# Kernel tuning notes

Hardware: AMD Instinct MI355X
Metric: run time of the kernel (lower is better)

The kernel has to match this reference:

```python
import jax, jax.numpy as jnp
import numpy as np

N = 50000
IN_C, HID_C, OUT_C = 128, 64, 32
E = 800000
NEG_SLOPE = 0.2


def setup_inputs() -> dict:
    key = jax.random.key(0)
    ks = jax.random.split(key, 8)
    x = jax.random.normal(ks[0], (N, IN_C), dtype=jnp.float32)
    edge_index = jax.random.randint(ks[1], (2, E), 0, N, dtype=jnp.int64)
    # GATConv params (heads=1): lin weight, att_src/att_dst vectors, bias
    sc = 1.0 / np.sqrt(IN_C)
    W = jax.random.uniform(ks[2], (IN_C, HID_C), jnp.float32, -sc, sc)
    att_src = jax.random.normal(ks[3], (HID_C,), jnp.float32) * (1.0 / np.sqrt(HID_C))
    att_dst = jax.random.normal(ks[4], (HID_C,), jnp.float32) * (1.0 / np.sqrt(HID_C))
    bias_conv = jnp.zeros((HID_C,), jnp.float32)
    sl = 1.0 / np.sqrt(HID_C)
    W_lin = jax.random.uniform(ks[5], (HID_C, OUT_C), jnp.float32, -sl, sl)
    b_lin = jax.random.uniform(ks[6], (OUT_C,), jnp.float32, -sl, sl)
    return {"x": x, "edge_index": edge_index, "W": W, "att_src": att_src,
            "att_dst": att_dst, "bias_conv": bias_conv, "W_lin": W_lin, "b_lin": b_lin}


def reference(x, edge_index, W, att_src, att_dst, bias_conv, W_lin, b_lin):
    n = x.shape[0]
    h = x @ W  # [N, HID]
    # add self-loops (PyG GATConv default add_self_loops=True)
    loop = jnp.arange(n, dtype=edge_index.dtype)
    src = jnp.concatenate([edge_index[0], loop])  # [E+N]
    dst = jnp.concatenate([edge_index[1], loop])
    a_src = h @ att_src  # [N]
    a_dst = h @ att_dst
    e = jax.nn.leaky_relu(a_src[src] + a_dst[dst], NEG_SLOPE)  # [E+N]
    # segment softmax over incoming edges per destination node
    m = jax.ops.segment_max(e, dst, num_segments=n)
    e = jnp.exp(e - m[dst])
    denom = jax.ops.segment_sum(e, dst, num_segments=n)
    alpha = e / (denom[dst] + 1e-16)
    msg = alpha[:, None] * h[src]  # [E+N, HID]
    out = jax.ops.segment_sum(msg, dst, num_segments=n) + bias_conv
    out = jax.nn.relu(out)
    return out @ W_lin + b_lin
```

## Files before the change

kernel.cpp:

```cpp
#include <hip/hip_runtime.h>
#include <hip/hip_bf16.h>

#define IN_C  128
#define HID_C 64
#define OUT_C 32
#define NEG_SLOPE 0.2f
#define EPB1    2048
#define BUCKETW 32
#define RCAP    768
#define SUPW    1024
#define RCAP1   18432
#define CSTRIDE 16
#define XS_LD   136

typedef short bf16x8 __attribute__((ext_vector_type(8)));
typedef float f32x4  __attribute__((ext_vector_type(4)));

__device__ __forceinline__ unsigned short f2bf(float f) {
    __hip_bfloat16 h = __float2bfloat16(f);
    return *(unsigned short*)&h;
}
__device__ __forceinline__ float bflo(unsigned int u) {
    return __uint_as_float(u << 16);
}
__device__ __forceinline__ float bfhi(unsigned int u) {
    return __uint_as_float(u & 0xffff0000u);
}

__global__ __launch_bounds__(256) void gemm_bin1_kernel(
    const float* __restrict__ x, const float* __restrict__ W,
    const float* __restrict__ att_src, const float* __restrict__ att_dst,
    __hip_bfloat16* __restrict__ hb,
    float* __restrict__ a_src, float* __restrict__ a_dst,
    const int* __restrict__ ei, int E,
    int* __restrict__ bcur1, unsigned* __restrict__ superbuf,
    int ngemm, int n_nodes)
{
    __shared__ __align__(16) unsigned char smem[34816];
    const int t = threadIdx.x;

    if ((int)blockIdx.x < ngemm) {
        unsigned short* xs = (unsigned short*)smem;
        unsigned short* wt = (unsigned short*)(smem + 17408);
        const int wv   = t >> 6;
        const int lane = t & 63;
        const int m16  = lane & 15;
        const int quad = lane >> 4;
        const int node0 = blockIdx.x * 64;
        const int nrows = min(64, n_nodes - node0);

        {
            const float4* xg = (const float4*)(x + (long)node0 * IN_C);
#pragma unroll
            for (int i = t; i < 2048; i += 256) {
                const int row = i >> 5;
                const int c4  = i & 31;
                float4 v = (row < nrows) ? xg[i] : make_float4(0.f, 0.f, 0.f, 0.f);
                ushort4 u;
                u.x = f2bf(v.x); u.y = f2bf(v.y);
                u.z = f2bf(v.z); u.w = f2bf(v.w);
                *(ushort4*)(xs + row * XS_LD + c4 * 4) = u;
            }
        }
        {
#pragma unroll
            for (int i = t; i < 2048; i += 256) {
                const int k  = i >> 4;
                const int n0 = (i & 15) * 4;
                const float4 v = *(const float4*)(W + k * HID_C + n0);
                wt[(n0 + 0) * XS_LD + k] = f2bf(v.x);
                wt[(n0 + 1) * XS_LD + k] = f2bf(v.y);
                wt[(n0 + 2) * XS_LD + k] = f2bf(v.z);
                wt[(n0 + 3) * XS_LD + k] = f2bf(v.w);
            }
        }
        __syncthreads();

        const int myrow0 = wv * 16;
        bf16x8 A[4];
#pragma unroll
        for (int k0 = 0; k0 < 4; ++k0)
            A[k0] = *(const bf16x8*)(xs + (myrow0 + m16) * XS_LD + k0 * 32 + quad * 8);

        f32x4 C[4];
#pragma unroll
        for (int c = 0; c < 4; ++c) {
            C[c] = (f32x4){0.f, 0.f, 0.f, 0.f};
#pragma unroll
            for (int k0 = 0; k0 < 4; ++k0) {
                const bf16x8 B = *(const bf16x8*)(wt + (c * 16 + m16) * XS_LD + k0 * 32 + quad * 8);
                C[c] = __builtin_amdgcn_mfma_f32_16x16x32_bf16(A[k0], B, C[c], 0, 0, 0);
            }
        }

#pragma unroll
        for (int c = 0; c < 4; ++c) {
#pragma unroll
            for (int r = 0; r < 4; ++r) {
                const int row = myrow0 + quad * 4 + r;
                if (row < nrows)
                    hb[(long)(node0 + row) * HID_C + c * 16 + m16] = __float2bfloat16(C[c][r]);
            }
        }

        {
            float ps[4] = {0.f, 0.f, 0.f, 0.f};
            float pd[4] = {0.f, 0.f, 0.f, 0.f};
#pragma unroll
            for (int c = 0; c < 4; ++c) {
                const float av = att_src[c * 16 + m16];
                const float dv = att_dst[c * 16 + m16];
#pragma unroll
                for (int r = 0; r < 4; ++r) {
                    ps[r] = fmaf(C[c][r], av, ps[r]);
                    pd[r] = fmaf(C[c][r], dv, pd[r]);
                }
            }
#pragma unroll
            for (int off = 1; off <= 8; off <<= 1) {
#pragma unroll
                for (int r = 0; r < 4; ++r) {
                    ps[r] += __shfl_xor(ps[r], off, 64);
                    pd[r] += __shfl_xor(pd[r], off, 64);
                }
            }
            if (m16 == 0) {
#pragma unroll
                for (int r = 0; r < 4; ++r) {
                    const int row = myrow0 + quad * 4 + r;
                    if (row < nrows) {
                        a_src[node0 + row] = ps[r];
                        a_dst[node0 + row] = pd[r];
                    }
                }
            }
        }
    } else {
        unsigned* stage = (unsigned*)smem;
        int* excl = (int*)(smem + 8192);
        int* cur  = (int*)(smem + 8448);
        int* gpos = (int*)(smem + 8704);

        const int base = (blockIdx.x - ngemm) * EPB1;
        const int nedge = min(EPB1, E - base);

        if (t < 64) excl[t] = 0;
        __syncthreads();

        for (int i = t; i < nedge; i += 256)
            atomicAdd(&excl[ei[E + base + i] >> 10], 1);
        __syncthreads();

        if (t < 64) {
            int c = excl[t], incl = c;
#pragma unroll
            for (int off = 1; off <= 32; off <<= 1) {
                int u = __shfl_up(incl, off, 64);
                if (t >= off) incl += u;
            }
            excl[t] = incl - c;
            cur[t]  = incl - c;
        }
        __syncthreads();

        for (int i = t; i < nedge; i += 256) {
            const int s = ei[base + i];
            const int d = ei[E + base + i];
            const int sq = d >> 10;
            const int pos = atomicAdd(&cur[sq], 1);
            stage[pos] = (unsigned)s | ((unsigned)(d & 1023) << 16)
                         | ((unsigned)sq << 26);
        }
        __syncthreads();

        if (t < 64) {
            const int c = cur[t] - excl[t];
            gpos[t] = (c > 0) ? atomicAdd(&bcur1[t * CSTRIDE], c) : 0;
        }
        __syncthreads();

        for (int i = t; i < nedge; i += 256) {
            const unsigned r = stage[i];
            const int sq = r >> 26;
            const int dp = gpos[sq] + (i - excl[sq]);
            if (dp < RCAP1) superbuf[(long)sq * RCAP1 + dp] = r;
        }
    }
}

__global__ __launch_bounds__(256) void agg_kernel(
    const unsigned* __restrict__ superbuf, const int* __restrict__ bcur1,
    const __hip_bfloat16* __restrict__ hb,
    const float* __restrict__ a_src, const float* __restrict__ a_dst,
    const float* __restrict__ bias_conv,
    const float* __restrict__ W_lin, const float* __restrict__ b_lin,
    float* __restrict__ out, int n_nodes)
{
    __shared__ unsigned lst[RCAP];
    __shared__ unsigned srtL[RCAP];
    __shared__ int lcnt;
    __shared__ int cntd[BUCKETW];
    __shared__ int rp[BUCKETW + 1];
    __shared__ int curd[BUCKETW];

    const int t  = threadIdx.x;
    const int q  = blockIdx.x;
    const int d0 = q * BUCKETW;
    const int dmax = min(BUCKETW, n_nodes - d0);
    const int sq   = q >> 5;
    const int ridx = q & 31;
    const int tot1 = min(bcur1[sq * CSTRIDE], RCAP1);
    const int wv = t >> 6, lane = t & 63, g8 = lane >> 3, l = lane & 7;

    if (t < BUCKETW) cntd[t] = 0;
    if (t == 0) lcnt = 0;
    __syncthreads();

    {
        const unsigned* sb = superbuf + (long)sq * RCAP1;
        for (int i0 = t * 4; i0 < tot1; i0 += 1024) {
            const uint4 v = *(const uint4*)(sb + i0);
            const unsigned rr[4] = {v.x, v.y, v.z, v.w};
#pragma unroll
            for (int k = 0; k < 4; ++k) {
                const unsigned r = rr[k];
                const bool ok = (i0 + k < tot1) && ((((r >> 21) ^ (unsigned)ridx) & 31u) == 0u);
                if (ok) {
                    const int pos = atomicAdd(&lcnt, 1);
                    if (pos < RCAP) {
                        lst[pos] = r & 0x1FFFFFu;
                        atomicAdd(&cntd[(r >> 16) & 31], 1);
                    }
                }
            }
        }
    }
    __syncthreads();

    const int nl = min(lcnt, RCAP);

    if (t < 32) {
        int c = cntd[t], incl = c;
#pragma unroll
        for (int off = 1; off <= 16; off <<= 1) {
            int u = __shfl_up(incl, off, 64);
            if (t >= off) incl += u;
        }
        rp[t] = incl - c;
        curd[t] = incl - c;
        if (t == 31) rp[32] = incl;
    }
    __syncthreads();

    for (int i = t; i < nl; i += 256) {
        const unsigned r = lst[i];
        const int pos = atomicAdd(&curd[(r >> 16) & 31], 1);
        srtL[pos] = r;
    }
    __syncthreads();

    float Wr[8][4];
#pragma unroll
    for (int kc = 0; kc < 8; ++kc)
#pragma unroll
        for (int kj = 0; kj < 4; ++kj)
            Wr[kc][kj] = W_lin[(l * 8 + kc) * OUT_C + g8 * 4 + kj];
    float biasR[8];
#pragma unroll
    for (int kc = 0; kc < 8; ++kc) biasR[kc] = bias_conv[l * 8 + kc];
    float blinR[4];
#pragma unroll
    for (int kj = 0; kj < 4; ++kj) blinR[kj] = b_lin[g8 * 4 + kj];

    const unsigned short* hbs = (const unsigned short*)hb;

    for (int dloc = wv; dloc < dmax; dloc += 4) {
        const int d = d0 + dloc;
        const float ad = a_dst[d];
        float A[8] = {0.f,0.f,0.f,0.f,0.f,0.f,0.f,0.f};
        float den = 0.f;
        if (g8 == 0) {
            float e = a_src[d] + ad;
            e = (e >= 0.f) ? e : NEG_SLOPE * e;
            const float ws = __expf(e);
            const uint4 hv = *(const uint4*)(hbs + (long)d * HID_C + l * 8);
            den = ws;
            A[0] = ws * bflo(hv.x); A[1] = ws * bfhi(hv.x);
            A[2] = ws * bflo(hv.y); A[3] = ws * bfhi(hv.y);
            A[4] = ws * bflo(hv.z); A[5] = ws * bfhi(hv.z);
            A[6] = ws * bflo(hv.w); A[7] = ws * bfhi(hv.w);
        }
        const int beg = rp[dloc], fin = rp[dloc + 1];
        for (int j = beg + g8; j < fin; j += 16) {
            const int  j1   = j + 8;
            const bool has1 = j1 < fin;
            const unsigned r0 = srtL[j];
            const unsigned r1 = srtL[has1 ? j1 : j];
            const int   s0 = r0 & 0xFFFF;
            const int   s1 = r1 & 0xFFFF;
            const float as0 = a_src[s0];
            const float as1 = a_src[s1];
            const uint4 h0 = *(const uint4*)(hbs + (long)s0 * HID_C + l * 8);
            const uint4 h1 = *(const uint4*)(hbs + (long)s1 * HID_C + l * 8);
            float e0 = as0 + ad; e0 = (e0 >= 0.f) ? e0 : NEG_SLOPE * e0;
            float e1 = as1 + ad; e1 = (e1 >= 0.f) ? e1 : NEG_SLOPE * e1;
            const float w0 = __expf(e0);
            const float w1 = has1 ? __expf(e1) : 0.f;
            den += w0 + w1;
            A[0] = fmaf(w0, bflo(h0.x), A[0]); A[1] = fmaf(w0, bfhi(h0.x), A[1]);
            A[2] = fmaf(w0, bflo(h0.y), A[2]); A[3] = fmaf(w0, bfhi(h0.y), A[3]);
            A[4] = fmaf(w0, bflo(h0.z), A[4]); A[5] = fmaf(w0, bfhi(h0.z), A[5]);
            A[6] = fmaf(w0, bflo(h0.w), A[6]); A[7] = fmaf(w0, bfhi(h0.w), A[7]);
            A[0] = fmaf(w1, bflo(h1.x), A[0]); A[1] = fmaf(w1, bfhi(h1.x), A[1]);
            A[2] = fmaf(w1, bflo(h1.y), A[2]); A[3] = fmaf(w1, bfhi(h1.y), A[3]);
            A[4] = fmaf(w1, bflo(h1.z), A[4]); A[5] = fmaf(w1, bfhi(h1.z), A[5]);
            A[6] = fmaf(w1, bflo(h1.w), A[6]); A[7] = fmaf(w1, bfhi(h1.w), A[7]);
        }
#pragma unroll
        for (int off = 8; off <= 32; off <<= 1) {
#pragma unroll
            for (int k = 0; k < 8; ++k) A[k] += __shfl_xor(A[k], off, 64);
            den += __shfl_xor(den, off, 64);
        }
        const float rd = 1.0f / (den + 1e-16f);
        float p0 = 0.f, p1 = 0.f, p2 = 0.f, p3 = 0.f;
#pragma unroll
        for (int kc = 0; kc < 8; ++kc) {
            float vv = fmaf(A[kc], rd, biasR[kc]);
            vv = vv > 0.f ? vv : 0.f;
            p0 = fmaf(vv, Wr[kc][0], p0);
            p1 = fmaf(vv, Wr[kc][1], p1);
            p2 = fmaf(vv, Wr[kc][2], p2);
            p3 = fmaf(vv, Wr[kc][3], p3);
        }
#pragma unroll
        for (int off = 1; off <= 4; off <<= 1) {
            p0 += __shfl_xor(p0, off, 64);
            p1 += __shfl_xor(p1, off, 64);
            p2 += __shfl_xor(p2, off, 64);
            p3 += __shfl_xor(p3, off, 64);
        }
        if (l == 0) {
            float4 o = make_float4(p0 + blinR[0], p1 + blinR[1],
                                   p2 + blinR[2], p3 + blinR[3]);
            *(float4*)(out + (long)d * OUT_C + g8 * 4) = o;
        }
    }
}

extern "C" void kernel_launch(void* const* d_in, const int* in_sizes, int n_in,
                              void* d_out, int out_size, void* d_ws, size_t ws_size,
                              hipStream_t stream) {
    const float* x         = (const float*)d_in[0];
    const int*   ei        = (const int*)d_in[1];
    const float* W         = (const float*)d_in[2];
    const float* att_src   = (const float*)d_in[3];
    const float* att_dst   = (const float*)d_in[4];
    const float* bias_conv = (const float*)d_in[5];
    const float* W_lin     = (const float*)d_in[6];
    const float* b_lin     = (const float*)d_in[7];
    float*       out       = (float*)d_out;

    const int n_nodes = in_sizes[0] / IN_C;
    const int E       = in_sizes[1] / 2;
    const int B1   = (E + EPB1 - 1) / EPB1;
    const int Q    = (n_nodes + BUCKETW - 1) / BUCKETW;
    const int NSUP = (n_nodes + SUPW - 1) / SUPW;
    const int NG   = (n_nodes + 63) / 64;

    __hip_bfloat16* hb = (__hip_bfloat16*)d_ws;
    float* a_src   = (float*)(hb + (long)n_nodes * HID_C);
    float* a_dst   = a_src + n_nodes;
    int*   bcur1   = (int*)(a_dst + n_nodes);
    unsigned* superbuf = (unsigned*)(bcur1 + (long)NSUP * CSTRIDE);

    hipMemsetAsync(bcur1, 0, (size_t)NSUP * CSTRIDE * sizeof(int), stream);

    gemm_bin1_kernel<<<NG + B1, 256, 0, stream>>>(
        x, W, att_src, att_dst, hb, a_src, a_dst,
        ei, E, bcur1, superbuf, NG, n_nodes);

    agg_kernel<<<Q, 256, 0, stream>>>(
        superbuf, bcur1, hb, a_src, a_dst,
        bias_conv, W_lin, b_lin, out, n_nodes);
}
```

Baseline: 161.8 us.

## Bin edges directly into 64-node buckets instead of 1024-node superbuckets

The binning pass now scatters edges straight into 1024 fine buckets of 64 destination nodes each, using a block-wide prefix scan over 1024 counters. The aggregation kernel then reads only its own bucket, so each block no longer scans a whole superbucket and filters out edges that belong to other blocks. The aggregation kernel also moves to 512 threads with 64 destinations per block. In exchange there are more global atomics on bucket cursors, a larger shared-memory scan, fewer and bigger aggregation blocks, and a per-bucket capacity of 1536 edges that silently drops overflow.

Result: no change. 161.5 us (-0.2%).

```diff
diff --git a/kernel.cpp b/kernel.cpp
--- a/kernel.cpp
+++ b/kernel.cpp
@@ -6,10 +6,9 @@
 #define OUT_C 32
 #define NEG_SLOPE 0.2f
 #define EPB1    2048
-#define BUCKETW 32
-#define RCAP    768
-#define SUPW    1024
-#define RCAP1   18432
+#define BUCKETW 64
+#define RCAP    1536
+#define NBKT    1024
 #define CSTRIDE 16
 #define XS_LD   136
 
@@ -33,7 +32,7 @@
     __hip_bfloat16* __restrict__ hb,
     float* __restrict__ a_src, float* __restrict__ a_dst,
     const int* __restrict__ ei, int E,
-    int* __restrict__ bcur1, unsigned* __restrict__ superbuf,
+    int* __restrict__ bcur, unsigned* __restrict__ bucketbuf,
     int ngemm, int n_nodes)
 {
     __shared__ __align__(16) unsigned char smem[34816];
@@ -138,67 +137,78 @@
     } else {
         unsigned* stage = (unsigned*)smem;
         int* excl = (int*)(smem + 8192);
-        int* cur  = (int*)(smem + 8448);
-        int* gpos = (int*)(smem + 8704);
+        int* cur  = (int*)(smem + 12288);
+        int* gpos = (int*)(smem + 16384);
+        int* wsum = (int*)(smem + 20480);
 
         const int base = (blockIdx.x - ngemm) * EPB1;
         const int nedge = min(EPB1, E - base);
-
-        if (t < 64) excl[t] = 0;
+        const int lane = t & 63, wv = t >> 6;
+
+        for (int i = t; i < NBKT; i += 256) excl[i] = 0;
         __syncthreads();
 
         for (int i = t; i < nedge; i += 256)
-            atomicAdd(&excl[ei[E + base + i] >> 10], 1);
-        __syncthreads();
-
-        if (t < 64) {
-            int c = excl[t], incl = c;
+            atomicAdd(&excl[ei[E + base + i] >> 6], 1);
+        __syncthreads();
+
+        {
+            const int b0 = t * 4;
+            const int c0 = excl[b0], c1 = excl[b0 + 1], c2 = excl[b0 + 2], c3 = excl[b0 + 3];
+            const int tsum = c0 + c1 + c2 + c3;
+            int incl = tsum;
 #pragma unroll
             for (int off = 1; off <= 32; off <<= 1) {
                 int u = __shfl_up(incl, off, 64);
-                if (t >= off) incl += u;
-            }
-            excl[t] = incl - c;
-            cur[t]  = incl - c;
+                if (lane >= off) incl += u;
+            }
+            if (lane == 63) wsum[wv] = incl;
+            __syncthreads();
+            int wbase = 0;
+#pragma unroll
+            for (int w = 0; w < 4; ++w) wbase += (w < wv) ? wsum[w] : 0;
+            int run = wbase + (incl - tsum);
+            excl[b0]     = run; cur[b0]     = run; run += c0;
+            excl[b0 + 1] = run; cur[b0 + 1] = run; run += c1;
+            excl[b0 + 2] = run; cur[b0 + 2] = run; run += c2;
+            excl[b0 + 3] = run; cur[b0 + 3] = run;
         }
         __syncthreads();
 
         for (int i = t; i < nedge; i += 256) {
             const int s = ei[base + i];
             const int d = ei[E + base + i];
-            const int sq = d >> 10;
-            const int pos = atomicAdd(&cur[sq], 1);
-            stage[pos] = (unsigned)s | ((unsigned)(d & 1023) << 16)
-                         | ((unsigned)sq << 26);
-        }
-        __syncthreads();
-
-        if (t < 64) {
-            const int c = cur[t] - excl[t];
-            gpos[t] = (c > 0) ? atomicAdd(&bcur1[t * CSTRIDE], c) : 0;
+            const int b = d >> 6;
+            const int pos = atomicAdd(&cur[b], 1);
+            stage[pos] = (unsigned)s | ((unsigned)(d & 63) << 16)
+                         | ((unsigned)b << 22);
+        }
+        __syncthreads();
+
+        for (int b = t; b < NBKT; b += 256) {
+            const int c = cur[b] - excl[b];
+            gpos[b] = (c > 0) ? atomicAdd(&bcur[b * CSTRIDE], c) : 0;
         }
         __syncthreads();
 
         for (int i = t; i < nedge; i += 256) {
             const unsigned r = stage[i];
-            const int sq = r >> 26;
-            const int dp = gpos[sq] + (i - excl[sq]);
-            if (dp < RCAP1) superbuf[(long)sq * RCAP1 + dp] = r;
+            const int b = r >> 22;
+            const int dp = gpos[b] + (i - excl[b]);
+            if (dp < RCAP) bucketbuf[(long)b * RCAP + dp] = r & 0x3FFFFFu;
         }
     }
 }
 
-__global__ __launch_bounds__(256) void agg_kernel(
-    const unsigned* __restrict__ superbuf, const int* __restrict__ bcur1,
+__global__ __launch_bounds__(512) void bucket_agg_kernel(
+    const unsigned* __restrict__ bucketbuf, const int* __restrict__ bcursor,
     const __hip_bfloat16* __restrict__ hb,
     const float* __restrict__ a_src, const float* __restrict__ a_dst,
     const float* __restrict__ bias_conv,
     const float* __restrict__ W_lin, const float* __restrict__ b_lin,
     float* __restrict__ out, int n_nodes)
 {
-    __shared__ unsigned lst[RCAP];
     __shared__ unsigned srtL[RCAP];
-    __shared__ int lcnt;
     __shared__ int cntd[BUCKETW];
     __shared__ int rp[BUCKETW + 1];
     __shared__ int curd[BUCKETW];
@@ -207,54 +217,34 @@
     const int q  = blockIdx.x;
     const int d0 = q * BUCKETW;
     const int dmax = min(BUCKETW, n_nodes - d0);
-    const int sq   = q >> 5;
-    const int ridx = q & 31;
-    const int tot1 = min(bcur1[sq * CSTRIDE], RCAP1);
+    const int tot  = min(bcursor[q * CSTRIDE], RCAP);
     const int wv = t >> 6, lane = t & 63, g8 = lane >> 3, l = lane & 7;
 
     if (t < BUCKETW) cntd[t] = 0;
-    if (t == 0) lcnt = 0;
     __syncthreads();
 
-    {
-        const unsigned* sb = superbuf + (long)sq * RCAP1;
-        for (int i0 = t * 4; i0 < tot1; i0 += 1024) {
-            const uint4 v = *(const uint4*)(sb + i0);
-            const unsigned rr[4] = {v.x, v.y, v.z, v.w};
-#pragma unroll
-            for (int k = 0; k < 4; ++k) {
-                const unsigned r = rr[k];
-                const bool ok = (i0 + k < tot1) && ((((r >> 21) ^ (unsigned)ridx) & 31u) == 0u);
-                if (ok) {
-                    const int pos = atomicAdd(&lcnt, 1);
-                    if (pos < RCAP) {
-                        lst[pos] = r & 0x1FFFFFu;
-                        atomicAdd(&cntd[(r >> 16) & 31], 1);
-                    }
-                }
-            }
-        }
+    const unsigned* gsrc = bucketbuf + (long)q * RCAP;
+
+    for (int i = t; i < tot; i += 512)
+        atomicAdd(&cntd[(gsrc[i] >> 16) & 63], 1);
+    __syncthreads();
+
+    if (t < 64) {
+        int c = cntd[t], incl = c;
+#pragma unroll
+        for (int off = 1; off <= 32; off <<= 1) {
+            int u = __shfl_up(incl, off, 64);
+            if (t >= off) incl += u;
+        }
+        rp[t] = incl - c;
+        curd[t] = incl - c;
+        if (t == 63) rp[64] = incl;
     }
     __syncthreads();
 
-    const int nl = min(lcnt, RCAP);
-
-    if (t < 32) {
-        int c = cntd[t], incl = c;
-#pragma unroll
-        for (int off = 1; off <= 16; off <<= 1) {
-            int u = __shfl_up(incl, off, 64);
-            if (t >= off) incl += u;
-        }
-        rp[t] = incl - c;
-        curd[t] = incl - c;
-        if (t == 31) rp[32] = incl;
-    }
-    __syncthreads();
-
-    for (int i = t; i < nl; i += 256) {
-        const unsigned r = lst[i];
-        const int pos = atomicAdd(&curd[(r >> 16) & 31], 1);
+    for (int i = t; i < tot; i += 512) {
+        const unsigned r = gsrc[i];
+        const int pos = atomicAdd(&curd[(r >> 16) & 63], 1);
         srtL[pos] = r;
     }
     __syncthreads();
@@ -274,7 +264,7 @@
 
     const unsigned short* hbs = (const unsigned short*)hb;
 
-    for (int dloc = wv; dloc < dmax; dloc += 4) {
+    for (int dloc = wv; dloc < dmax; dloc += 8) {
         const int d = d0 + dloc;
         const float ad = a_dst[d];
         float A[8] = {0.f,0.f,0.f,0.f,0.f,0.f,0.f,0.f};
@@ -365,22 +355,21 @@
     const int E       = in_sizes[1] / 2;
     const int B1   = (E + EPB1 - 1) / EPB1;
     const int Q    = (n_nodes + BUCKETW - 1) / BUCKETW;
-    const int NSUP = (n_nodes + SUPW - 1) / SUPW;
     const int NG   = (n_nodes + 63) / 64;
 
     __hip_bfloat16* hb = (__hip_bfloat16*)d_ws;
     float* a_src   = (float*)(hb + (long)n_nodes * HID_C);
     float* a_dst   = a_src + n_nodes;
-    int*   bcur1   = (int*)(a_dst + n_nodes);
-    unsigned* superbuf = (unsigned*)(bcur1 + (long)NSUP * CSTRIDE);
-
-    hipMemsetAsync(bcur1, 0, (size_t)NSUP * CSTRIDE * sizeof(int), stream);
+    int*   bcur    = (int*)(a_dst + n_nodes);
+    unsigned* bucketbuf = (unsigned*)(bcur + (long)Q * CSTRIDE);
+
+    hipMemsetAsync(bcur, 0, (size_t)Q * CSTRIDE * sizeof(int), stream);
 
     gemm_bin1_kernel<<<NG + B1, 256, 0, stream>>>(
         x, W, att_src, att_dst, hb, a_src, a_dst,
-        ei, E, bcur1, superbuf, NG, n_nodes);
-
-    agg_kernel<<<Q, 256, 0, stream>>>(
-        superbuf, bcur1, hb, a_src, a_dst,
+        ei, E, bcur, bucketbuf, NG, n_nodes);
+
+    bucket_agg_kernel<<<Q, 512, 0, stream>>>(
+        bucketbuf, bcur, hb, a_src, a_dst,
         bias_conv, W_lin, b_lin, out, n_nodes);
 }
```
